# Kernel optimization log

Hardware: AMD Instinct MI355X
Metric: run time of the kernel (lower is better)

Reference implementation:

```python
import jax, jax.numpy as jnp
import numpy as np

N, DIM, NH, HD, M = 2048, 1024, 16, 64, 2
LN_EPS = 1e-5


def setup_inputs() -> dict:
    key = jax.random.key(0)
    ks = jax.random.split(key, 8)
    x = jax.random.normal(ks[0], (N, DIM), dtype=jnp.float32)
    ids = jax.random.randint(ks[1], (N,), 0, M)
    modality_masks = jnp.stack([ids == m for m in range(M)])  # [M, N] bool partition
    s = 0.02
    wq = jax.random.normal(ks[2], (M, DIM, NH * HD), dtype=jnp.float32) * s
    wk = jax.random.normal(ks[3], (M, DIM, NH * HD), dtype=jnp.float32) * s
    wv = jax.random.normal(ks[4], (M, DIM, NH * HD), dtype=jnp.float32) * s
    wo = jax.random.normal(ks[5], (M, NH * HD, DIM), dtype=jnp.float32) * s
    ln_w = jnp.ones((M, DIM), dtype=jnp.float32)
    ln_b = jnp.zeros((M, DIM), dtype=jnp.float32)
    return dict(x=x, modality_masks=modality_masks, n_heads=NH,
                wq=wq, wk=wk, wv=wv, wo=wo, ln_w=ln_w, ln_b=ln_b)


def reference(x, modality_masks, n_heads, wq, wk, wv, wo, ln_w, ln_b):
    # x: [N, dim]; modality_masks: [M, N] bool (partition of tokens)
    n_mod, n_tok = modality_masks.shape
    hd = wq.shape[-1] // n_heads
    scale = hd ** -0.5

    mod_id = jnp.argmax(modality_masks, axis=0)          # [N] modality of each token
    perm = jnp.argsort(mod_id, stable=True)              # concat order: mod-0 tokens, then mod-1, ...
    xp = x[perm]                                          # gathered tokens in expert order
    oh = jax.nn.one_hot(mod_id[perm], n_mod, dtype=x.dtype)  # [N, M] expert selector

    def expert_proj(inp, w):
        # inp: [N, din], w: [M, din, dout] -> per-token output using that token's expert
        all_out = jnp.einsum('nd,mdo->mno', inp, w)       # [M, N, dout]
        return jnp.einsum('nm,mno->no', oh, all_out)      # select expert per token

    q = expert_proj(xp, wq).reshape(n_tok, n_heads, hd).transpose(1, 0, 2)  # [H, N, hd]
    k = expert_proj(xp, wk).reshape(n_tok, n_heads, hd).transpose(1, 0, 2)
    v = expert_proj(xp, wv).reshape(n_tok, n_heads, hd).transpose(1, 0, 2)

    scores = jnp.einsum('hnd,hkd->hnk', q, k) * scale     # [H, N, N] full attention over merged tokens
    probs = jax.nn.softmax(scores, axis=-1)
    attn = jnp.einsum('hnk,hkd->hnd', probs, v)           # [H, N, hd]
    attn = attn.transpose(1, 0, 2).reshape(n_tok, n_heads * hd)

    o = expert_proj(attn, wo)                              # [N, dim] per-modality wo
    mu = jnp.mean(o, axis=-1, keepdims=True)
    var = jnp.mean((o - mu) ** 2, axis=-1, keepdims=True)
    on = (o - mu) * jax.lax.rsqrt(var + LN_EPS)
    g = oh @ ln_w                                          # [N, dim] per-token LN scale
    b = oh @ ln_b
    out_perm = on * g + b

    out = jnp.zeros_like(x).at[perm].set(out_perm)         # scatter back to original order
    return out
```

## Files before the change

kernel.cpp:

```cpp
#include <hip/hip_runtime.h>

typedef __attribute__((ext_vector_type(8))) short short8v;
typedef __attribute__((ext_vector_type(4))) float f32x4;
typedef __attribute__((ext_vector_type(16))) float f32x16;
typedef unsigned short u16;
typedef unsigned int u32;

#define MFMA __builtin_amdgcn_mfma_f32_16x16x32_bf16
#define MFMA32 __builtin_amdgcn_mfma_f32_32x32x16_bf16

__device__ __forceinline__ u16 f2b(float f) {
  u32 u = __float_as_uint(f);
  u = (u + 0x7FFFu + ((u >> 16) & 1u)) >> 16;
  return (u16)u;
}
__device__ __forceinline__ float b2f(u16 b) {
  return __uint_as_float(((u32)b) << 16);
}
__device__ __forceinline__ void g2l16(const void* g, void* l) {
  __builtin_amdgcn_global_load_lds(
      (const __attribute__((address_space(1))) unsigned int*)g,
      (__attribute__((address_space(3))) unsigned int*)l, 16, 0, 0);
}

#define N_TOK 2048
#define DIM 1024
#define NH 16
#define HD 64

#define QSCALE 0.18033688011112042f

#define OFF_PERM 0
#define OFF_CNT 8192
#define OFF_XPB 16384
#define OFF_WT (OFF_XPB + 4194304)
#define OFF_Q (OFF_WT + 16777216)
#define OFF_K (OFF_Q + 4194304)
#define OFF_V (OFF_K + 4194304)
#define OFF_VT (OFF_V + 4194304)
#define OFF_AT (OFF_VT + 4194304)
#define OFF_O (OFF_AT + 4194304)

__global__ __launch_bounds__(256) void prep_kernel(const void* __restrict__ masks,
                                                   int* __restrict__ perm,
                                                   int* __restrict__ cnt) {
  const int tid = threadIdx.x;
  __shared__ u32 red[256];
  __shared__ int scan[256];
  const u32* mw = (const u32*)masks;
  u32 mx = 0;
  for (int i = tid; i < 1024; i += 256) { u32 v = mw[i]; mx = mx > v ? mx : v; }
  red[tid] = mx;
  __syncthreads();
  for (int off = 128; off; off >>= 1) {
    if (tid < off) red[tid] = red[tid] > red[tid + off] ? red[tid] : red[tid + off];
    __syncthreads();
  }
  const bool isbyte = red[0] > 1u;
  int md[8];
  int c0loc = 0;
  #pragma unroll
  for (int j = 0; j < 8; ++j) {
    const int n = tid * 8 + j;
    int m1;
    if (isbyte) m1 = ((const unsigned char*)masks)[N_TOK + n] != 0;
    else        m1 = mw[N_TOK + n] != 0;
    md[j] = m1;
    c0loc += (m1 == 0);
  }
  scan[tid] = c0loc;
  __syncthreads();
  for (int off = 1; off < 256; off <<= 1) {
    int v = (tid >= off) ? scan[tid - off] : 0;
    __syncthreads();
    scan[tid] += v;
    __syncthreads();
  }
  const int incl = scan[tid];
  const int total0 = scan[255];
  const int excl0 = incl - c0loc;
  int p0 = excl0;
  int p1 = total0 + (tid * 8 - excl0);
  #pragma unroll
  for (int j = 0; j < 8; ++j) {
    const int n = tid * 8 + j;
    if (!md[j]) perm[p0++] = n; else perm[p1++] = n;
  }
  if (tid == 0) cnt[0] = total0;
}

__global__ __launch_bounds__(256) void gather_cast(const float* __restrict__ x,
                                                   const int* __restrict__ perm,
                                                   u16* __restrict__ xpb) {
  const int i = blockIdx.x;
  const int src = perm[i];
  const int tid = threadIdx.x;
  float4 v = ((const float4*)(x + (size_t)src * DIM))[tid];
  ushort4 o;
  o.x = f2b(v.x); o.y = f2b(v.y); o.z = f2b(v.z); o.w = f2b(v.w);
  ((ushort4*)(xpb + (size_t)i * DIM))[tid] = o;
}

__global__ __launch_bounds__(256) void wcast(const float* __restrict__ wq,
                                             const float* __restrict__ wk,
                                             const float* __restrict__ wv,
                                             const float* __restrict__ wo,
                                             u16* __restrict__ wT) {
  const int mat = blockIdx.z;
  const int tensor = mat >> 1, expert = mat & 1;
  const float* src = (tensor == 0) ? wq : (tensor == 1) ? wk : (tensor == 2) ? wv : wo;
  src += (size_t)expert * (1 << 20);
  u16* dst = wT + ((size_t)mat << 20);
  const int k0 = blockIdx.x * 32, n0 = blockIdx.y * 32;
  const int tx = threadIdx.x, ty = threadIdx.y;
  __shared__ float t[32][33];
  #pragma unroll
  for (int r = 0; r < 4; ++r)
    t[ty + 8 * r][tx] = src[(size_t)(k0 + ty + 8 * r) * DIM + n0 + tx];
  __syncthreads();
  #pragma unroll
  for (int r = 0; r < 4; ++r)
    dst[(size_t)(n0 + ty + 8 * r) * DIM + k0 + tx] = f2b(t[tx][ty + 8 * r]);
}

__global__ __launch_bounds__(256) void vtrans(const u16* __restrict__ v,
                                              u16* __restrict__ vT) {
  const int h = blockIdx.z;
  const int n0 = blockIdx.x * 32, d0 = blockIdx.y * 32;
  const int tx = threadIdx.x, ty = threadIdx.y;
  __shared__ u16 t[32][33];
  #pragma unroll
  for (int r = 0; r < 4; ++r)
    t[ty + 8 * r][tx] = v[(size_t)(n0 + ty + 8 * r) * DIM + h * HD + d0 + tx];
  __syncthreads();
  #pragma unroll
  for (int r = 0; r < 4; ++r)
    vT[(size_t)(h * HD + d0 + ty + 8 * r) * N_TOK + n0 + tx] = t[tx][ty + 8 * r];
}

template <int OUTF32>
__global__ __launch_bounds__(256) void gemm_exp(const u16* __restrict__ X,
                                                const u16* __restrict__ WTall,
                                                int tensor0, float scale0,
                                                void* __restrict__ o0,
                                                void* __restrict__ o1,
                                                void* __restrict__ o2,
                                                const int* __restrict__ cntp) {
  const int z = blockIdx.z;
  const int e = blockIdx.y >> 4;
  const int mt = blockIdx.y & 15;
  const int c0 = cntp[0];
  const int lo = e ? c0 : 0;
  const int hi = e ? N_TOK : c0;
  const int rb = mt * 128;
  if (rb >= hi || rb + 128 <= lo) return;
  const int cb = blockIdx.x * 128;
  void* OUT = (z == 0) ? o0 : (z == 1) ? o1 : o2;
  const u16* W = WTall + ((size_t)((tensor0 + z) * 2 + e) << 20);
  const float scl = (z == 0) ? scale0 : 1.f;

  const int tid = threadIdx.x;
  const int w = tid >> 6, l = tid & 63, lg = l >> 4, ln = l & 15;
  const int wm = (w >> 1) * 64, wn = (w & 1) * 64;

  __shared__ __align__(16) char smem[32768];

  auto stage = [&](int it, int b_) {
    const int k0b = it * 64;
    #pragma unroll
    for (int c = 0; c < 2; ++c) {
      const int lb = (tid + c * 256) * 16;
      const int row = lb >> 6, colb = lb & 63;
      g2l16((const char*)X + (size_t)(rb + row) * 2048 + k0b + colb,
            &smem[b_ * 16384 + lb]);
      g2l16((const char*)W + (size_t)(cb + row) * 2048 + k0b + colb,
            &smem[b_ * 16384 + 8192 + lb]);
    }
  };

  f32x4 acc[4][4];
  #pragma unroll
  for (int i = 0; i < 4; ++i)
    #pragma unroll
    for (int j = 0; j < 4; ++j) acc[i][j] = (f32x4){0.f, 0.f, 0.f, 0.f};

  stage(0, 0);
  __syncthreads();
  for (int it = 0; it < 32; ++it) {
    const int b_ = it & 1;
    if (it < 31) stage(it + 1, b_ ^ 1);
    short8v a[4], bb[4];
    #pragma unroll
    for (int mi = 0; mi < 4; ++mi)
      a[mi] = *(const short8v*)&smem[b_ * 16384 + (wm + mi * 16 + ln) * 64 + lg * 16];
    #pragma unroll
    for (int ni = 0; ni < 4; ++ni)
      bb[ni] = *(const short8v*)&smem[b_ * 16384 + 8192 + (wn + ni * 16 + ln) * 64 + lg * 16];
    __builtin_amdgcn_s_setprio(1);
    #pragma unroll
    for (int mi = 0; mi < 4; ++mi)
      #pragma unroll
      for (int ni = 0; ni < 4; ++ni)
        acc[mi][ni] = MFMA(a[mi], bb[ni], acc[mi][ni], 0, 0, 0);
    __builtin_amdgcn_s_setprio(0);
    __syncthreads();
  }

  #pragma unroll
  for (int mi = 0; mi < 4; ++mi) {
    #pragma unroll
    for (int r = 0; r < 4; ++r) {
      const int row = rb + wm + mi * 16 + lg * 4 + r;
      if (row >= lo && row < hi) {
        #pragma unroll
        for (int ni = 0; ni < 4; ++ni) {
          const int col = cb + wn + ni * 16 + ln;
          const float vv = acc[mi][ni][r] * scl;
          if (OUTF32) ((float*)OUT)[(size_t)row * DIM + col] = vv;
          else ((u16*)OUT)[(size_t)row * DIM + col] = f2b(vv);
        }
      }
    }
  }
}

__global__ __launch_bounds__(256, 2) void attn_fwd(const u16* __restrict__ qg,
                                                   const u16* __restrict__ kg,
                                                   const u16* __restrict__ vTg,
                                                   u16* __restrict__ og) {
  const int qt = blockIdx.x, h = blockIdx.y;
  const int tid = threadIdx.x, w = tid >> 6, l = tid & 63;
  const int g = w & 1, kh = w >> 1;
  const int q31 = l & 31;
  const int hi = l >> 5;
  const int hi16 = hi * 16, hi4 = hi * 4;

  __shared__ __align__(16) char smem[65536];

  auto stage = [&](int it, int b_) {
    #pragma unroll
    for (int c = 0; c < 8; ++c) {
      const int j = tid + c * 256;
      const int s_ = j >> 10;
      const int rem = j & 1023;
      const int isV = rem >> 9;
      const int cc = rem & 511;
      const int r = cc >> 3, c16 = cc & 7;
      const int colb = (c16 * 16) ^ ((r & 7) << 4);
      const char* src;
      if (isV)
        src = (const char*)vTg + (size_t)(h * HD + r) * 4096 + (s_ * 1024 + it * 64) * 2 + colb;
      else
        src = (const char*)kg + (size_t)(s_ * 1024 + it * 64 + r) * 2048 + h * 128 + colb;
      g2l16(src, &smem[s_ * 32768 + b_ * 16384 + isV * 8192 + cc * 16]);
    }
  };
  auto ldf = [&](int base, int row, int colb) -> short8v {
    return *(const short8v*)&smem[base + row * 128 + (colb ^ ((row & 7) << 4))];
  };

  const char* qrow = (const char*)qg + ((size_t)(qt * 64 + g * 32 + q31)) * 2048 + h * 128;
  short8v qf[4];
  #pragma unroll
  for (int t = 0; t < 4; ++t) qf[t] = *(const short8v*)(qrow + t * 32 + hi16);

  stage(0, 0);
  __syncthreads();

  float m_s = -1e30f, l_s = 0.f;
  f32x16 accO[2];
  #pragma unroll
  for (int dt = 0; dt < 2; ++dt)
    #pragma unroll
    for (int r = 0; r < 16; ++r) accO[dt][r] = 0.f;

  for (int it = 0; it < 16; ++it) {
    const int b_ = it & 1;
    if (it < 15) stage(it + 1, b_ ^ 1);
    const int Kb = kh * 32768 + b_ * 16384;
    const int Vb = Kb + 8192;

    #pragma unroll
    for (int ks = 0; ks < 2; ++ks) {
      f32x16 s_;
      #pragma unroll
      for (int r = 0; r < 16; ++r) s_[r] = 0.f;
      {
        short8v kf0 = ldf(Kb, ks * 32 + q31, 0 * 32 + hi16);
        short8v kf1 = ldf(Kb, ks * 32 + q31, 1 * 32 + hi16);
        short8v kf2 = ldf(Kb, ks * 32 + q31, 2 * 32 + hi16);
        short8v kf3 = ldf(Kb, ks * 32 + q31, 3 * 32 + hi16);
        __builtin_amdgcn_s_setprio(1);
        s_ = MFMA32(kf0, qf[0], s_, 0, 0, 0);
        s_ = MFMA32(kf1, qf[1], s_, 0, 0, 0);
        s_ = MFMA32(kf2, qf[2], s_, 0, 0, 0);
        s_ = MFMA32(kf3, qf[3], s_, 0, 0, 0);
        __builtin_amdgcn_s_setprio(0);
      }

      float tmax = s_[0];
      #pragma unroll
      for (int r = 1; r < 16; ++r) tmax = fmaxf(tmax, s_[r]);
      tmax = fmaxf(tmax, __shfl_xor(tmax, 32, 64));

      if (!__all(tmax <= m_s + 11.0f)) {
        const float mn = fmaxf(m_s, tmax);
        const float al = __builtin_amdgcn_exp2f(m_s - mn);
        m_s = mn;
        l_s *= al;
        #pragma unroll
        for (int r = 0; r < 16; ++r) {
          const float ar = __shfl(al, (r & 3) + 8 * (r >> 2) + hi4, 64);
          accO[0][r] *= ar;
          accO[1][r] *= ar;
        }
      }

      float p[16];
      float rs = 0.f;
      #pragma unroll
      for (int r = 0; r < 16; ++r) {
        p[r] = __builtin_amdgcn_exp2f(s_[r] - m_s);
        rs += p[r];
      }
      rs += __shfl_xor(rs, 32, 64);
      l_s += rs;

      u32 c0, c1, c2, c3, c4, c5, c6, c7;
      asm("v_cvt_pk_bf16_f32 %0, %1, %2" : "=v"(c0) : "v"(p[0]), "v"(p[1]));
      asm("v_cvt_pk_bf16_f32 %0, %1, %2" : "=v"(c1) : "v"(p[2]), "v"(p[3]));
      asm("v_cvt_pk_bf16_f32 %0, %1, %2" : "=v"(c2) : "v"(p[4]), "v"(p[5]));
      asm("v_cvt_pk_bf16_f32 %0, %1, %2" : "=v"(c3) : "v"(p[6]), "v"(p[7]));
      asm("v_cvt_pk_bf16_f32 %0, %1, %2" : "=v"(c4) : "v"(p[8]), "v"(p[9]));
      asm("v_cvt_pk_bf16_f32 %0, %1, %2" : "=v"(c5) : "v"(p[10]), "v"(p[11]));
      asm("v_cvt_pk_bf16_f32 %0, %1, %2" : "=v"(c6) : "v"(p[12]), "v"(p[13]));
      asm("v_cvt_pk_bf16_f32 %0, %1, %2" : "=v"(c7) : "v"(p[14]), "v"(p[15]));
      asm volatile("v_permlane32_swap_b32 %0, %1" : "+v"(c0), "+v"(c2));
      asm volatile("v_permlane32_swap_b32 %0, %1" : "+v"(c1), "+v"(c3));
      asm volatile("v_permlane32_swap_b32 %0, %1" : "+v"(c4), "+v"(c6));
      asm volatile("v_permlane32_swap_b32 %0, %1" : "+v"(c5), "+v"(c7));
      union { u32 u[4]; short8v s; } pa0, pa1;
      pa0.u[0] = c0; pa0.u[1] = c1; pa0.u[2] = c2; pa0.u[3] = c3;
      pa1.u[0] = c4; pa1.u[1] = c5; pa1.u[2] = c6; pa1.u[3] = c7;

      #pragma unroll
      for (int kk = 0; kk < 2; ++kk) {
        const short8v pa = kk ? pa1.s : pa0.s;
        short8v vb0 = ldf(Vb, q31, ks * 64 + kk * 32 + hi16);
        short8v vb1 = ldf(Vb, 32 + q31, ks * 64 + kk * 32 + hi16);
        __builtin_amdgcn_s_setprio(1);
        accO[0] = MFMA32(pa, vb0, accO[0], 0, 0, 0);
        accO[1] = MFMA32(pa, vb1, accO[1], 0, 0, 0);
        __builtin_amdgcn_s_setprio(0);
      }
    }
    __syncthreads();
  }

  float* mlds = (float*)&smem[32768];
  if (l < 32) {
    mlds[(g * 2 + kh) * 32 + l] = m_s;
    mlds[128 + (g * 2 + kh) * 32 + l] = l_s;
  }
  __syncthreads();
  const float m0 = mlds[(g * 2 + 0) * 32 + q31];
  const float m1 = mlds[(g * 2 + 1) * 32 + q31];
  const float l0 = mlds[128 + (g * 2 + 0) * 32 + q31];
  const float l1 = mlds[128 + (g * 2 + 1) * 32 + q31];
  const float M = fmaxf(m0, m1);
  const float a0 = __builtin_amdgcn_exp2f(m0 - M);
  const float a1 = __builtin_amdgcn_exp2f(m1 - M);
  const float linv = 1.f / (l0 * a0 + l1 * a1);
  const float aown = kh ? a1 : a0;
  float* obuf = (float*)&smem[0];
  if (kh == 1) {
    #pragma unroll
    for (int r = 0; r < 16; ++r) {
      const int qr = (r & 3) + 8 * (r >> 2) + hi4;
      const float ar = __shfl(aown, qr, 64);
      obuf[(g * 32 + qr) * 64 + q31] = accO[0][r] * ar;
      obuf[(g * 32 + qr) * 64 + 32 + q31] = accO[1][r] * ar;
    }
  }
  __syncthreads();
  if (kh == 0) {
    #pragma unroll
    for (int r = 0; r < 16; ++r) {
      const int qr = (r & 3) + 8 * (r >> 2) + hi4;
      const float ar = __shfl(aown, qr, 64);
      const float li = __shfl(linv, qr, 64);
      const int row = qt * 64 + g * 32 + qr;
      const float v0 = (accO[0][r] * ar + obuf[(g * 32 + qr) * 64 + q31]) * li;
      const float v1 = (accO[1][r] * ar + obuf[(g * 32 + qr) * 64 + 32 + q31]) * li;
      og[(size_t)row * DIM + h * HD + q31] = f2b(v0);
      og[(size_t)row * DIM + h * HD + 32 + q31] = f2b(v1);
    }
  }
}

__global__ __launch_bounds__(256) void ln_scatter(const float* __restrict__ o,
                                                  const float* __restrict__ lnw,
                                                  const float* __restrict__ lnb,
                                                  const int* __restrict__ perm,
                                                  const int* __restrict__ cntp,
                                                  float* __restrict__ out) {
  const int i = blockIdx.x;
  const int tid = threadIdx.x, w = tid >> 6, l = tid & 63;
  const int mod = (i < cntp[0]) ? 0 : 1;
  float4 v = ((const float4*)(o + (size_t)i * DIM))[tid];
  float s = v.x + v.y + v.z + v.w;
  float ss = v.x * v.x + v.y * v.y + v.z * v.z + v.w * v.w;
  #pragma unroll
  for (int off = 1; off < 64; off <<= 1) {
    s += __shfl_xor(s, off, 64);
    ss += __shfl_xor(ss, off, 64);
  }
  __shared__ float rs4[4], rss4[4];
  if (l == 0) { rs4[w] = s; rss4[w] = ss; }
  __syncthreads();
  const float st = rs4[0] + rs4[1] + rs4[2] + rs4[3];
  const float sst = rss4[0] + rss4[1] + rss4[2] + rss4[3];
  const float mu = st * (1.f / DIM);
  const float var = sst * (1.f / DIM) - mu * mu;
  const float rstd = rsqrtf(var + 1e-5f);
  const int drow = perm[i];
  float4 g = ((const float4*)(lnw + (size_t)mod * DIM))[tid];
  float4 b = ((const float4*)(lnb + (size_t)mod * DIM))[tid];
  float4 rr;
  rr.x = (v.x - mu) * rstd * g.x + b.x;
  rr.y = (v.y - mu) * rstd * g.y + b.y;
  rr.z = (v.z - mu) * rstd * g.z + b.z;
  rr.w = (v.w - mu) * rstd * g.w + b.w;
  ((float4*)(out + (size_t)drow * DIM))[tid] = rr;
}

extern "C" void kernel_launch(void* const* d_in, const int* in_sizes, int n_in,
                              void* d_out, int out_size, void* d_ws, size_t ws_size,
                              hipStream_t stream) {
  const float* x = (const float*)d_in[0];
  const void* masks = d_in[1];
  const float* wq = (const float*)d_in[3];
  const float* wk = (const float*)d_in[4];
  const float* wv = (const float*)d_in[5];
  const float* wo = (const float*)d_in[6];
  const float* lnw = (const float*)d_in[7];
  const float* lnb = (const float*)d_in[8];

  char* ws = (char*)d_ws;
  int* perm = (int*)(ws + OFF_PERM);
  int* cnt = (int*)(ws + OFF_CNT);
  u16* xpb = (u16*)(ws + OFF_XPB);
  u16* wT = (u16*)(ws + OFF_WT);
  u16* q = (u16*)(ws + OFF_Q);
  u16* k = (u16*)(ws + OFF_K);
  u16* v = (u16*)(ws + OFF_V);
  u16* vT = (u16*)(ws + OFF_VT);
  u16* at = (u16*)(ws + OFF_AT);
  float* o = (float*)(ws + OFF_O);
  float* out = (float*)d_out;

  prep_kernel<<<1, 256, 0, stream>>>(masks, perm, cnt);
  gather_cast<<<N_TOK, 256, 0, stream>>>(x, perm, xpb);
  wcast<<<dim3(32, 32, 8), dim3(32, 8), 0, stream>>>(wq, wk, wv, wo, wT);
  gemm_exp<0><<<dim3(8, 32, 3), 256, 0, stream>>>(xpb, wT, 0, QSCALE, q, k, v, cnt);
  vtrans<<<dim3(64, 2, 16), dim3(32, 8), 0, stream>>>(v, vT);
  attn_fwd<<<dim3(32, 16), 256, 0, stream>>>(q, k, vT, at);
  gemm_exp<1><<<dim3(8, 32, 1), 256, 0, stream>>>(at, wT, 3, 1.0f, o, o, o, cnt);
  ln_scatter<<<N_TOK, 256, 0, stream>>>(o, lnw, lnb, perm, cnt, out);
}
```

Measured before the change: 111.0 us.

## Split attention keys across four waves per query tile and split-K the output projection

The attention kernel moves from 256 to 512 threads, with four key-split wave groups each handling 32-key tiles instead of two groups of 64. The partial softmax states are merged through a staged LDS reduction, and blocks are remapped to interleave heads and query tiles. The output projection GEMM is split over K into two halves written to separate fp32 buffers, and the LayerNorm kernel sums them. This aims to raise occupancy and parallelism in both stages, at the cost of an extra 8MB partial buffer, more reduction rounds with barriers, and more LDS traffic.

```diff
diff --git a/kernel.cpp b/kernel.cpp
--- a/kernel.cpp
+++ b/kernel.cpp
@@ -40,6 +40,7 @@
 #define OFF_VT (OFF_V + 4194304)
 #define OFF_AT (OFF_VT + 4194304)
 #define OFF_O (OFF_AT + 4194304)
+#define OFF_O2 (OFF_O + 8388608)
 
 __global__ __launch_bounds__(256) void prep_kernel(const void* __restrict__ masks,
                                                    int* __restrict__ perm,
@@ -142,6 +143,7 @@
 __global__ __launch_bounds__(256) void gemm_exp(const u16* __restrict__ X,
                                                 const u16* __restrict__ WTall,
                                                 int tensor0, float scale0,
+                                                int split_k,
                                                 void* __restrict__ o0,
                                                 void* __restrict__ o1,
                                                 void* __restrict__ o2,
@@ -155,9 +157,16 @@
   const int rb = mt * 128;
   if (rb >= hi || rb + 128 <= lo) return;
   const int cb = blockIdx.x * 128;
-  void* OUT = (z == 0) ? o0 : (z == 1) ? o1 : o2;
-  const u16* W = WTall + ((size_t)((tensor0 + z) * 2 + e) << 20);
-  const float scl = (z == 0) ? scale0 : 1.f;
+  int tensor, kstart, kiters;
+  void* OUT;
+  float scl;
+  if (split_k) {
+    tensor = tensor0; OUT = z ? o1 : o0; kstart = z * 16; kiters = 16; scl = 1.f;
+  } else {
+    tensor = tensor0 + z; OUT = (z == 0) ? o0 : (z == 1) ? o1 : o2;
+    kstart = 0; kiters = 32; scl = (z == 0) ? scale0 : 1.f;
+  }
+  const u16* W = WTall + ((size_t)(tensor * 2 + e) << 20);
 
   const int tid = threadIdx.x;
   const int w = tid >> 6, l = tid & 63, lg = l >> 4, ln = l & 15;
@@ -184,11 +193,11 @@
     #pragma unroll
     for (int j = 0; j < 4; ++j) acc[i][j] = (f32x4){0.f, 0.f, 0.f, 0.f};
 
-  stage(0, 0);
-  __syncthreads();
-  for (int it = 0; it < 32; ++it) {
-    const int b_ = it & 1;
-    if (it < 31) stage(it + 1, b_ ^ 1);
+  stage(kstart, 0);
+  __syncthreads();
+  for (int ii = 0; ii < kiters; ++ii) {
+    const int b_ = ii & 1;
+    if (ii < kiters - 1) stage(kstart + ii + 1, b_ ^ 1);
     short8v a[4], bb[4];
     #pragma unroll
     for (int mi = 0; mi < 4; ++mi)
@@ -224,42 +233,43 @@
   }
 }
 
-__global__ __launch_bounds__(256, 2) void attn_fwd(const u16* __restrict__ qg,
+__global__ __launch_bounds__(512, 4) void attn_fwd(const u16* __restrict__ qg,
                                                    const u16* __restrict__ kg,
                                                    const u16* __restrict__ vTg,
                                                    u16* __restrict__ og) {
-  const int qt = blockIdx.x, h = blockIdx.y;
+  const int bid = blockIdx.x;
+  const int wg = (bid & 7) * 64 + (bid >> 3);
+  const int qt = wg & 31, h = wg >> 5;
   const int tid = threadIdx.x, w = tid >> 6, l = tid & 63;
-  const int g = w & 1, kh = w >> 1;
-  const int q31 = l & 31;
-  const int hi = l >> 5;
+  const int g = w & 1, kq = w >> 1;
+  const int q31 = l & 31, hi = l >> 5;
   const int hi16 = hi * 16, hi4 = hi * 4;
 
   __shared__ __align__(16) char smem[65536];
 
   auto stage = [&](int it, int b_) {
     #pragma unroll
-    for (int c = 0; c < 8; ++c) {
-      const int j = tid + c * 256;
-      const int s_ = j >> 10;
-      const int rem = j & 1023;
-      const int isV = rem >> 9;
-      const int cc = rem & 511;
-      const int r = cc >> 3, c16 = cc & 7;
-      const int colb = (c16 * 16) ^ ((r & 7) << 4);
+    for (int c = 0; c < 4; ++c) {
+      const int j = tid + c * 512;
+      const int s_ = j >> 9;
+      const int rem = j & 511;
+      const int isV = rem >> 8;
+      const int cc = rem & 255;
       const char* src;
-      if (isV)
-        src = (const char*)vTg + (size_t)(h * HD + r) * 4096 + (s_ * 1024 + it * 64) * 2 + colb;
-      else
-        src = (const char*)kg + (size_t)(s_ * 1024 + it * 64 + r) * 2048 + h * 128 + colb;
-      g2l16(src, &smem[s_ * 32768 + b_ * 16384 + isV * 8192 + cc * 16]);
+      if (isV) {
+        const int r = cc >> 2, c16 = cc & 3;
+        const int colb = (c16 * 16) ^ (((r >> 2) & 3) << 4);
+        src = (const char*)vTg + (size_t)(h * HD + r) * 4096 + s_ * 1024 + it * 64 + colb;
+      } else {
+        const int r = cc >> 3, c16 = cc & 7;
+        const int colb = (c16 * 16) ^ ((r & 7) << 4);
+        src = (const char*)kg + (size_t)(s_ * 512 + it * 32 + r) * 2048 + h * 128 + colb;
+      }
+      g2l16(src, &smem[s_ * 16384 + b_ * 8192 + isV * 4096 + cc * 16]);
     }
   };
-  auto ldf = [&](int base, int row, int colb) -> short8v {
-    return *(const short8v*)&smem[base + row * 128 + (colb ^ ((row & 7) << 4))];
-  };
-
-  const char* qrow = (const char*)qg + ((size_t)(qt * 64 + g * 32 + q31)) * 2048 + h * 128;
+
+  const char* qrow = (const char*)qg + (size_t)(qt * 64 + g * 32 + q31) * 2048 + h * 128;
   short8v qf[4];
   #pragma unroll
   for (int t = 0; t < 4; ++t) qf[t] = *(const short8v*)(qrow + t * 32 + hi16);
@@ -270,135 +280,139 @@
   float m_s = -1e30f, l_s = 0.f;
   f32x16 accO[2];
   #pragma unroll
-  for (int dt = 0; dt < 2; ++dt)
-    #pragma unroll
-    for (int r = 0; r < 16; ++r) accO[dt][r] = 0.f;
+  for (int ds = 0; ds < 2; ++ds)
+    #pragma unroll
+    for (int r = 0; r < 16; ++r) accO[ds][r] = 0.f;
+
+  const int kswz = (q31 & 7) << 4;
+  const int vswz = ((q31 >> 2) & 3) << 4;
 
   for (int it = 0; it < 16; ++it) {
     const int b_ = it & 1;
     if (it < 15) stage(it + 1, b_ ^ 1);
-    const int Kb = kh * 32768 + b_ * 16384;
-    const int Vb = Kb + 8192;
-
-    #pragma unroll
-    for (int ks = 0; ks < 2; ++ks) {
-      f32x16 s_;
+    const int Kb = kq * 16384 + b_ * 8192;
+    const int Vb = Kb + 4096;
+
+    short8v kf[4];
+    #pragma unroll
+    for (int t = 0; t < 4; ++t)
+      kf[t] = *(const short8v*)&smem[Kb + q31 * 128 + ((t * 32 + hi16) ^ kswz)];
+    f32x16 s_;
+    #pragma unroll
+    for (int r = 0; r < 16; ++r) s_[r] = 0.f;
+    __builtin_amdgcn_s_setprio(1);
+    s_ = MFMA32(kf[0], qf[0], s_, 0, 0, 0);
+    s_ = MFMA32(kf[1], qf[1], s_, 0, 0, 0);
+    s_ = MFMA32(kf[2], qf[2], s_, 0, 0, 0);
+    s_ = MFMA32(kf[3], qf[3], s_, 0, 0, 0);
+    __builtin_amdgcn_s_setprio(0);
+
+    float a0 = fmaxf(fmaxf(s_[0], s_[1]), fmaxf(s_[2], s_[3]));
+    float a1 = fmaxf(fmaxf(s_[4], s_[5]), fmaxf(s_[6], s_[7]));
+    float a2 = fmaxf(fmaxf(s_[8], s_[9]), fmaxf(s_[10], s_[11]));
+    float a3 = fmaxf(fmaxf(s_[12], s_[13]), fmaxf(s_[14], s_[15]));
+    float tmax = fmaxf(fmaxf(a0, a1), fmaxf(a2, a3));
+    tmax = fmaxf(tmax, __shfl_xor(tmax, 32, 64));
+
+    if (!__all(tmax <= m_s + 11.0f)) {
+      const float mn = fmaxf(m_s, tmax);
+      const float al = __builtin_amdgcn_exp2f(m_s - mn);
+      m_s = mn;
+      l_s *= al;
       #pragma unroll
-      for (int r = 0; r < 16; ++r) s_[r] = 0.f;
-      {
-        short8v kf0 = ldf(Kb, ks * 32 + q31, 0 * 32 + hi16);
-        short8v kf1 = ldf(Kb, ks * 32 + q31, 1 * 32 + hi16);
-        short8v kf2 = ldf(Kb, ks * 32 + q31, 2 * 32 + hi16);
-        short8v kf3 = ldf(Kb, ks * 32 + q31, 3 * 32 + hi16);
-        __builtin_amdgcn_s_setprio(1);
-        s_ = MFMA32(kf0, qf[0], s_, 0, 0, 0);
-        s_ = MFMA32(kf1, qf[1], s_, 0, 0, 0);
-        s_ = MFMA32(kf2, qf[2], s_, 0, 0, 0);
-        s_ = MFMA32(kf3, qf[3], s_, 0, 0, 0);
-        __builtin_amdgcn_s_setprio(0);
+      for (int r = 0; r < 16; ++r) {
+        const float ar = __shfl(al, (r & 3) + 8 * (r >> 2) + hi4, 64);
+        accO[0][r] *= ar;
+        accO[1][r] *= ar;
       }
-
-      float tmax = s_[0];
+    }
+
+    float p[16];
+    #pragma unroll
+    for (int r = 0; r < 16; ++r) p[r] = __builtin_amdgcn_exp2f(s_[r] - m_s);
+    float rs = ((p[0] + p[1]) + (p[2] + p[3])) + ((p[4] + p[5]) + (p[6] + p[7])) +
+               (((p[8] + p[9]) + (p[10] + p[11])) + ((p[12] + p[13]) + (p[14] + p[15])));
+    rs += __shfl_xor(rs, 32, 64);
+    l_s += rs;
+
+    u32 c0, c1, c2, c3, c4, c5, c6, c7;
+    asm("v_cvt_pk_bf16_f32 %0, %1, %2" : "=v"(c0) : "v"(p[0]), "v"(p[1]));
+    asm("v_cvt_pk_bf16_f32 %0, %1, %2" : "=v"(c1) : "v"(p[2]), "v"(p[3]));
+    asm("v_cvt_pk_bf16_f32 %0, %1, %2" : "=v"(c2) : "v"(p[4]), "v"(p[5]));
+    asm("v_cvt_pk_bf16_f32 %0, %1, %2" : "=v"(c3) : "v"(p[6]), "v"(p[7]));
+    asm("v_cvt_pk_bf16_f32 %0, %1, %2" : "=v"(c4) : "v"(p[8]), "v"(p[9]));
+    asm("v_cvt_pk_bf16_f32 %0, %1, %2" : "=v"(c5) : "v"(p[10]), "v"(p[11]));
+    asm("v_cvt_pk_bf16_f32 %0, %1, %2" : "=v"(c6) : "v"(p[12]), "v"(p[13]));
+    asm("v_cvt_pk_bf16_f32 %0, %1, %2" : "=v"(c7) : "v"(p[14]), "v"(p[15]));
+    asm volatile("v_permlane32_swap_b32 %0, %1" : "+v"(c0), "+v"(c2));
+    asm volatile("v_permlane32_swap_b32 %0, %1" : "+v"(c1), "+v"(c3));
+    asm volatile("v_permlane32_swap_b32 %0, %1" : "+v"(c4), "+v"(c6));
+    asm volatile("v_permlane32_swap_b32 %0, %1" : "+v"(c5), "+v"(c7));
+    union { u32 u[4]; short8v s; } pa0, pa1;
+    pa0.u[0] = c0; pa0.u[1] = c1; pa0.u[2] = c2; pa0.u[3] = c3;
+    pa1.u[0] = c4; pa1.u[1] = c5; pa1.u[2] = c6; pa1.u[3] = c7;
+
+    #pragma unroll
+    for (int kst = 0; kst < 2; ++kst) {
+      const short8v pa = kst ? pa1.s : pa0.s;
+      short8v vb0 = *(const short8v*)&smem[Vb + q31 * 64 + ((kst * 32 + hi16) ^ vswz)];
+      short8v vb1 = *(const short8v*)&smem[Vb + (32 + q31) * 64 + ((kst * 32 + hi16) ^ vswz)];
+      __builtin_amdgcn_s_setprio(1);
+      accO[0] = MFMA32(pa, vb0, accO[0], 0, 0, 0);
+      accO[1] = MFMA32(pa, vb1, accO[1], 0, 0, 0);
+      __builtin_amdgcn_s_setprio(0);
+    }
+    __syncthreads();
+  }
+
+  float* mm = (float*)&smem[32768];
+  if (l < 32) {
+    mm[(g * 4 + kq) * 32 + l] = m_s;
+    mm[256 + (g * 4 + kq) * 32 + l] = l_s;
+  }
+  __syncthreads();
+  float M = mm[(g * 4 + 0) * 32 + q31];
+  M = fmaxf(M, mm[(g * 4 + 1) * 32 + q31]);
+  M = fmaxf(M, mm[(g * 4 + 2) * 32 + q31]);
+  M = fmaxf(M, mm[(g * 4 + 3) * 32 + q31]);
+  float L = 0.f;
+  #pragma unroll
+  for (int j = 0; j < 4; ++j)
+    L += mm[256 + (g * 4 + j) * 32 + q31] *
+         __builtin_amdgcn_exp2f(mm[(g * 4 + j) * 32 + q31] - M);
+  const float aown = __builtin_amdgcn_exp2f(m_s - M);
+  const float linv = 1.f / L;
+
+  float* obuf = (float*)&smem[g * 8192];
+  #pragma unroll
+  for (int round = 3; round >= 0; --round) {
+    if (kq == round) {
       #pragma unroll
-      for (int r = 1; r < 16; ++r) tmax = fmaxf(tmax, s_[r]);
-      tmax = fmaxf(tmax, __shfl_xor(tmax, 32, 64));
-
-      if (!__all(tmax <= m_s + 11.0f)) {
-        const float mn = fmaxf(m_s, tmax);
-        const float al = __builtin_amdgcn_exp2f(m_s - mn);
-        m_s = mn;
-        l_s *= al;
-        #pragma unroll
-        for (int r = 0; r < 16; ++r) {
-          const float ar = __shfl(al, (r & 3) + 8 * (r >> 2) + hi4, 64);
-          accO[0][r] *= ar;
-          accO[1][r] *= ar;
+      for (int r = 0; r < 16; ++r) {
+        const int qr = (r & 3) + 8 * (r >> 2) + hi4;
+        const float ar = __shfl(aown, qr, 64);
+        float* p0 = &obuf[qr * 64 + q31];
+        float* p1 = &obuf[qr * 64 + 32 + q31];
+        if (round == 3) {
+          *p0 = accO[0][r] * ar;
+          *p1 = accO[1][r] * ar;
+        } else if (round > 0) {
+          *p0 += accO[0][r] * ar;
+          *p1 += accO[1][r] * ar;
+        } else {
+          const float li = __shfl(linv, qr, 64);
+          const int row = qt * 64 + g * 32 + qr;
+          og[(size_t)row * DIM + h * HD + q31] = f2b((accO[0][r] * ar + *p0) * li);
+          og[(size_t)row * DIM + h * HD + 32 + q31] = f2b((accO[1][r] * ar + *p1) * li);
         }
       }
-
-      float p[16];
-      float rs = 0.f;
-      #pragma unroll
-      for (int r = 0; r < 16; ++r) {
-        p[r] = __builtin_amdgcn_exp2f(s_[r] - m_s);
-        rs += p[r];
-      }
-      rs += __shfl_xor(rs, 32, 64);
-      l_s += rs;
-
-      u32 c0, c1, c2, c3, c4, c5, c6, c7;
-      asm("v_cvt_pk_bf16_f32 %0, %1, %2" : "=v"(c0) : "v"(p[0]), "v"(p[1]));
-      asm("v_cvt_pk_bf16_f32 %0, %1, %2" : "=v"(c1) : "v"(p[2]), "v"(p[3]));
-      asm("v_cvt_pk_bf16_f32 %0, %1, %2" : "=v"(c2) : "v"(p[4]), "v"(p[5]));
-      asm("v_cvt_pk_bf16_f32 %0, %1, %2" : "=v"(c3) : "v"(p[6]), "v"(p[7]));
-      asm("v_cvt_pk_bf16_f32 %0, %1, %2" : "=v"(c4) : "v"(p[8]), "v"(p[9]));
-      asm("v_cvt_pk_bf16_f32 %0, %1, %2" : "=v"(c5) : "v"(p[10]), "v"(p[11]));
-      asm("v_cvt_pk_bf16_f32 %0, %1, %2" : "=v"(c6) : "v"(p[12]), "v"(p[13]));
-      asm("v_cvt_pk_bf16_f32 %0, %1, %2" : "=v"(c7) : "v"(p[14]), "v"(p[15]));
-      asm volatile("v_permlane32_swap_b32 %0, %1" : "+v"(c0), "+v"(c2));
-      asm volatile("v_permlane32_swap_b32 %0, %1" : "+v"(c1), "+v"(c3));
-      asm volatile("v_permlane32_swap_b32 %0, %1" : "+v"(c4), "+v"(c6));
-      asm volatile("v_permlane32_swap_b32 %0, %1" : "+v"(c5), "+v"(c7));
-      union { u32 u[4]; short8v s; } pa0, pa1;
-      pa0.u[0] = c0; pa0.u[1] = c1; pa0.u[2] = c2; pa0.u[3] = c3;
-      pa1.u[0] = c4; pa1.u[1] = c5; pa1.u[2] = c6; pa1.u[3] = c7;
-
-      #pragma unroll
-      for (int kk = 0; kk < 2; ++kk) {
-        const short8v pa = kk ? pa1.s : pa0.s;
-        short8v vb0 = ldf(Vb, q31, ks * 64 + kk * 32 + hi16);
-        short8v vb1 = ldf(Vb, 32 + q31, ks * 64 + kk * 32 + hi16);
-        __builtin_amdgcn_s_setprio(1);
-        accO[0] = MFMA32(pa, vb0, accO[0], 0, 0, 0);
-        accO[1] = MFMA32(pa, vb1, accO[1], 0, 0, 0);
-        __builtin_amdgcn_s_setprio(0);
-      }
-    }
-    __syncthreads();
-  }
-
-  float* mlds = (float*)&smem[32768];
-  if (l < 32) {
-    mlds[(g * 2 + kh) * 32 + l] = m_s;
-    mlds[128 + (g * 2 + kh) * 32 + l] = l_s;
-  }
-  __syncthreads();
-  const float m0 = mlds[(g * 2 + 0) * 32 + q31];
-  const float m1 = mlds[(g * 2 + 1) * 32 + q31];
-  const float l0 = mlds[128 + (g * 2 + 0) * 32 + q31];
-  const float l1 = mlds[128 + (g * 2 + 1) * 32 + q31];
-  const float M = fmaxf(m0, m1);
-  const float a0 = __builtin_amdgcn_exp2f(m0 - M);
-  const float a1 = __builtin_amdgcn_exp2f(m1 - M);
-  const float linv = 1.f / (l0 * a0 + l1 * a1);
-  const float aown = kh ? a1 : a0;
-  float* obuf = (float*)&smem[0];
-  if (kh == 1) {
-    #pragma unroll
-    for (int r = 0; r < 16; ++r) {
-      const int qr = (r & 3) + 8 * (r >> 2) + hi4;
-      const float ar = __shfl(aown, qr, 64);
-      obuf[(g * 32 + qr) * 64 + q31] = accO[0][r] * ar;
-      obuf[(g * 32 + qr) * 64 + 32 + q31] = accO[1][r] * ar;
-    }
-  }
-  __syncthreads();
-  if (kh == 0) {
-    #pragma unroll
-    for (int r = 0; r < 16; ++r) {
-      const int qr = (r & 3) + 8 * (r >> 2) + hi4;
-      const float ar = __shfl(aown, qr, 64);
-      const float li = __shfl(linv, qr, 64);
-      const int row = qt * 64 + g * 32 + qr;
-      const float v0 = (accO[0][r] * ar + obuf[(g * 32 + qr) * 64 + q31]) * li;
-      const float v1 = (accO[1][r] * ar + obuf[(g * 32 + qr) * 64 + 32 + q31]) * li;
-      og[(size_t)row * DIM + h * HD + q31] = f2b(v0);
-      og[(size_t)row * DIM + h * HD + 32 + q31] = f2b(v1);
-    }
-  }
-}
-
-__global__ __launch_bounds__(256) void ln_scatter(const float* __restrict__ o,
+    }
+    __syncthreads();
+  }
+}
+
+__global__ __launch_bounds__(256) void ln_scatter(const float* __restrict__ oa,
+                                                  const float* __restrict__ ob,
                                                   const float* __restrict__ lnw,
                                                   const float* __restrict__ lnb,
                                                   const int* __restrict__ perm,
@@ -407,7 +421,10 @@
   const int i = blockIdx.x;
   const int tid = threadIdx.x, w = tid >> 6, l = tid & 63;
   const int mod = (i < cntp[0]) ? 0 : 1;
-  float4 v = ((const float4*)(o + (size_t)i * DIM))[tid];
+  float4 va = ((const float4*)(oa + (size_t)i * DIM))[tid];
+  float4 vb = ((const float4*)(ob + (size_t)i * DIM))[tid];
+  float4 v;
+  v.x = va.x + vb.x; v.y = va.y + vb.y; v.z = va.z + vb.z; v.w = va.w + vb.w;
   float s = v.x + v.y + v.z + v.w;
   float ss = v.x * v.x + v.y * v.y + v.z * v.z + v.w * v.w;
   #pragma unroll
@@ -457,14 +474,15 @@
   u16* vT = (u16*)(ws + OFF_VT);
   u16* at = (u16*)(ws + OFF_AT);
   float* o = (float*)(ws + OFF_O);
+  float* o2 = (float*)(ws + OFF_O2);
   float* out = (float*)d_out;
 
   prep_kernel<<<1, 256, 0, stream>>>(masks, perm, cnt);
   gather_cast<<<N_TOK, 256, 0, stream>>>(x, perm, xpb);
   wcast<<<dim3(32, 32, 8), dim3(32, 8), 0, stream>>>(wq, wk, wv, wo, wT);
-  gemm_exp<0><<<dim3(8, 32, 3), 256, 0, stream>>>(xpb, wT, 0, QSCALE, q, k, v, cnt);
+  gemm_exp<0><<<dim3(8, 32, 3), 256, 0, stream>>>(xpb, wT, 0, QSCALE, 0, q, k, v, cnt);
   vtrans<<<dim3(64, 2, 16), dim3(32, 8), 0, stream>>>(v, vT);
-  attn_fwd<<<dim3(32, 16), 256, 0, stream>>>(q, k, vT, at);
-  gemm_exp<1><<<dim3(8, 32, 1), 256, 0, stream>>>(at, wT, 3, 1.0f, o, o, o, cnt);
-  ln_scatter<<<N_TOK, 256, 0, stream>>>(o, lnw, lnb, perm, cnt, out);
-}
+  attn_fwd<<<512, 512, 0, stream>>>(q, k, vT, at);
+  gemm_exp<1><<<dim3(8, 32, 2), 256, 0, stream>>>(at, wT, 3, 1.0f, 1, o, o2, o, cnt);
+  ln_scatter<<<N_TOK, 256, 0, stream>>>(o, o2, lnw, lnb, perm, cnt, out);
+}
```

Result: faster. 107.3 us (-3.4%).
